# Kernel tuning notes

Hardware: AMD Instinct MI355X
Metric: run time of the kernel (lower is better)

Reference implementation:

```python
import jax, jax.numpy as jnp
import numpy as np

N_PRO = 100000
N_LIG = 100000
E = 500000
H = 128
CE = 18


def _lin_params(key, out_dim, in_dim, scale=0.02):
    kw, kb = jax.random.split(key)
    W = jax.random.normal(kw, (out_dim, in_dim), jnp.float32) * scale
    b = jax.random.normal(kb, (out_dim,), jnp.float32) * scale
    return W, b


def setup_inputs() -> dict:
    key = jax.random.key(0)
    ks = jax.random.split(key, 16)
    inp = {}
    inp['pro_x'] = jax.random.normal(ks[0], (N_PRO, H), jnp.float32)
    inp['lig_x'] = jax.random.normal(ks[1], (N_LIG, H), jnp.float32)
    pi = jax.random.randint(ks[2], (E,), 0, N_PRO)
    li = jax.random.randint(ks[3], (E,), 0, N_LIG)
    inp['cross_ei'] = jnp.stack([pi, li]).astype(jnp.int64)
    inp['cross_ea'] = jax.random.normal(ks[4], (E, CE), jnp.float32)
    inp['Wq_pro'], inp['bq_pro'] = _lin_params(ks[5], H, H)
    inp['Wk_lig'], inp['bk_lig'] = _lin_params(ks[6], H, H)
    inp['Wv_lig'], inp['bv_lig'] = _lin_params(ks[7], H, H)
    inp['Wq_lig'], inp['bq_lig'] = _lin_params(ks[8], H, H)
    inp['Wk_pro'], inp['bk_pro'] = _lin_params(ks[9], H, H)
    inp['Wv_pro'], inp['bv_pro'] = _lin_params(ks[10], H, H)
    inp['We_bias'] = jax.random.normal(ks[11], (CE,), jnp.float32) * 0.02  # Linear(CE,1,bias=False) weight
    inp['Wo_pro'], inp['bo_pro'] = _lin_params(ks[12], H, H)
    inp['Wo_lig'], inp['bo_lig'] = _lin_params(ks[13], H, H)
    inp['g_pro'] = jnp.ones((H,), jnp.float32)
    inp['be_pro'] = jnp.zeros((H,), jnp.float32)
    inp['g_lig'] = jnp.ones((H,), jnp.float32)
    inp['be_lig'] = jnp.zeros((H,), jnp.float32)
    return inp


def _layernorm(x, g, b, eps=1e-5):
    mu = jnp.mean(x, -1, keepdims=True)
    var = jnp.var(x, -1, keepdims=True)
    return (x - mu) * jax.lax.rsqrt(var + eps) * g + b


def _lin(x, W, b):
    return x @ W.T + b


def _attend(Q_src, K_tgt, V_tgt, bias, tgt_idx, n_tgt, scale):
    # per-edge score -> edge softmax over target nodes -> weighted scatter-add
    scores = jnp.sum(Q_src * K_tgt, -1) * scale + bias          # [E]
    scores = scores - jnp.max(scores)                            # global max, as in torch code
    exp_s = jnp.exp(scores)
    denom = jax.ops.segment_sum(exp_s, tgt_idx, num_segments=n_tgt)
    w = exp_s / (denom[tgt_idx] + 1e-8)                          # [E]
    return jax.ops.segment_sum(w[:, None] * V_tgt, tgt_idx, num_segments=n_tgt)  # [n_tgt, H]


def reference(pro_x, lig_x, cross_ei, cross_ea,
              Wq_pro, bq_pro, Wk_lig, bk_lig, Wv_lig, bv_lig,
              Wq_lig, bq_lig, Wk_pro, bk_pro, Wv_pro, bv_pro,
              We_bias, Wo_pro, bo_pro, Wo_lig, bo_lig,
              g_pro, be_pro, g_lig, be_lig):
    pi = cross_ei[0]
    li = cross_ei[1]
    h = pro_x.shape[1]
    scale = h ** (-0.5)
    bias = cross_ea @ We_bias                                    # [E]

    # protein <- ligand
    Qp = _lin(pro_x, Wq_pro, bq_pro)[pi]
    Kl = _lin(lig_x, Wk_lig, bk_lig)[li]
    Vl = _lin(lig_x, Wv_lig, bv_lig)[li]
    pro_upd = _attend(Qp, Kl, Vl, bias, pi, pro_x.shape[0], scale)
    pro_new = _layernorm(pro_x + _lin(pro_upd, Wo_pro, bo_pro), g_pro, be_pro)

    # ligand <- protein
    Ql = _lin(lig_x, Wq_lig, bq_lig)[li]
    Kp = _lin(pro_x, Wk_pro, bk_pro)[pi]
    Vp = _lin(pro_x, Wv_pro, bv_pro)[pi]
    lig_upd = _attend(Ql, Kp, Vp, bias, li, lig_x.shape[0], scale)
    lig_new = _layernorm(lig_x + _lin(lig_upd, Wo_lig, bo_lig), g_lig, be_lig)

    return (pro_new, lig_new)
```

## Files before the change

kernel.cpp:

```cpp
#include <hip/hip_runtime.h>
#include <float.h>
#include <math.h>


typedef __bf16 bf16x8 __attribute__((ext_vector_type(8)));
typedef float  f32x4  __attribute__((ext_vector_type(4)));
typedef float  f32x2  __attribute__((ext_vector_type(2)));
typedef unsigned int u32x2 __attribute__((ext_vector_type(2)));

__device__ __forceinline__ bf16x8 cvt8(const float* p) {
    f32x4 lo = *reinterpret_cast<const f32x4*>(p);
    f32x4 hi = *reinterpret_cast<const f32x4*>(p + 4);
    bf16x8 r;
    r[0] = (__bf16)lo[0]; r[1] = (__bf16)lo[1]; r[2] = (__bf16)lo[2]; r[3] = (__bf16)lo[3];
    r[4] = (__bf16)hi[0]; r[5] = (__bf16)hi[1]; r[6] = (__bf16)hi[2]; r[7] = (__bf16)hi[3];
    return r;
}

__device__ __forceinline__ u32x2 pack_fp8x8(const float* v) {
    int w0 = __builtin_amdgcn_cvt_pk_fp8_f32(v[0], v[1], 0, false);
    w0 = __builtin_amdgcn_cvt_pk_fp8_f32(v[2], v[3], w0, true);
    int w1 = __builtin_amdgcn_cvt_pk_fp8_f32(v[4], v[5], 0, false);
    w1 = __builtin_amdgcn_cvt_pk_fp8_f32(v[6], v[7], w1, true);
    u32x2 r; r[0] = (unsigned)w0; r[1] = (unsigned)w1;
    return r;
}

__device__ __forceinline__ void unpack_fp8x8(u32x2 p, float* out) {
    f32x2 t0 = __builtin_amdgcn_cvt_pk_f32_fp8((int)p[0], false);
    f32x2 t1 = __builtin_amdgcn_cvt_pk_f32_fp8((int)p[0], true);
    f32x2 t2 = __builtin_amdgcn_cvt_pk_f32_fp8((int)p[1], false);
    f32x2 t3 = __builtin_amdgcn_cvt_pk_f32_fp8((int)p[1], true);
    out[0] = t0[0]; out[1] = t0[1]; out[2] = t1[0]; out[3] = t1[1];
    out[4] = t2[0]; out[5] = t2[1]; out[6] = t3[0]; out[7] = t3[1];
}

__device__ __forceinline__ void stage_w512(const __bf16* __restrict__ Ws, char* wlds, int tid) {
#pragma unroll
    for (int it = 0; it < 4; ++it) {
        int idx = it * 4096 + tid * 8;
        int byteoff = idx * 2;
        int row = byteoff >> 8;
        *reinterpret_cast<bf16x8*>(wlds + (byteoff ^ ((row & 7) << 4)))
            = *reinterpret_cast<const bf16x8*>(Ws + idx);
    }
}
__device__ __forceinline__ bf16x8 read_w(const char* wlds, int l15, int lg, int ni, int ks) {
    int row = ni * 16 + l15;
    int off = (row * 256 + ks * 64 + lg * 16) ^ ((row & 7) << 4);
    return *reinterpret_cast<const bf16x8*>(wlds + off);
}

__global__ __launch_bounds__(256) void cvt_weights(
    const float* w0, const float* w1, const float* w2, const float* w3,
    const float* w4, const float* w5, const float* w6, const float* w7,
    __bf16* __restrict__ dst)
{
    const float* srcs[8] = {w0, w1, w2, w3, w4, w5, w6, w7};
    int t = blockIdx.x * 256 + threadIdx.x;
    int mat = t >> 11;
    int base = (t & 2047) * 8;
    const float* s = srcs[mat];
    bool perm = (mat == 3) || (mat == 7);
    __bf16* d = dst + (size_t)mat * 16384;
#pragma unroll
    for (int u = 0; u < 8; ++u) {
        int idx = base + u;
        int row = idx >> 7, c = idx & 127;
        int pos = perm ? ((c & 15) * 8 + (c >> 4)) : c;
        d[row * 128 + pos] = (__bf16)s[idx];
    }
}

__global__ __launch_bounds__(256) void bias_count(
    const float* __restrict__ ea, const float* __restrict__ We,
    const int* __restrict__ pi, const int* __restrict__ li,
    float* __restrict__ bias, int* __restrict__ counts,
    unsigned* __restrict__ ranks, int Np, int E, int CE)
{
    int e = blockIdx.x * 256 + threadIdx.x;
    if (e >= E) return;
    const float2* row = reinterpret_cast<const float2*>(ea + (size_t)e * CE);
    float acc = 0.f;
    int h = CE >> 1;
    for (int c = 0; c < h; ++c) {
        float2 v = row[c];
        acc += v.x * We[2 * c] + v.y * We[2 * c + 1];
    }
    if (CE & 1) acc += ea[(size_t)e * CE + CE - 1] * We[CE - 1];
    bias[e] = acc;
    int r0 = atomicAdd(&counts[pi[e]], 1);
    int r1 = atomicAdd(&counts[Np + li[e]], 1);
    ranks[e] = (unsigned)(r0 & 0xFFFF) | ((unsigned)r1 << 16);
}

__global__ __launch_bounds__(256) void scan1(
    const int* __restrict__ counts, int* __restrict__ offs,
    int* __restrict__ bsums, int N)
{
    int idx = blockIdx.x * 256 + threadIdx.x;
    int v = (idx < N) ? counts[idx] : 0;
    int lane = threadIdx.x & 63, w = threadIdx.x >> 6;
    int x = v;
#pragma unroll
    for (int d = 1; d < 64; d <<= 1) {
        int y = __shfl_up(x, d);
        if (lane >= d) x += y;
    }
    __shared__ int wsum[4];
    if (lane == 63) wsum[w] = x;
    __syncthreads();
    int add = 0;
    for (int i = 0; i < w; ++i) add += wsum[i];
    x += add;
    if (idx < N) offs[idx] = x - v;
    if (threadIdx.x == 255) bsums[blockIdx.x] = x;
}

__global__ __launch_bounds__(1024) void scan2(int* __restrict__ bsums, int nb)
{
    __shared__ int tmp[1024];
    int t = threadIdx.x;
    tmp[t] = (t < nb) ? bsums[t] : 0;
    __syncthreads();
    for (int d = 1; d < 1024; d <<= 1) {
        int y = (t >= d) ? tmp[t - d] : 0;
        __syncthreads();
        tmp[t] += y;
        __syncthreads();
    }
    if (t < nb) bsums[t] = tmp[t];
}

__global__ __launch_bounds__(256) void scan3(
    int* __restrict__ offs, const int* __restrict__ bsums, int N, int total)
{
    int idx = blockIdx.x * 256 + threadIdx.x;
    if (idx < N && blockIdx.x > 0) offs[idx] += bsums[blockIdx.x - 1];
    if (idx == 0) offs[N] = total;
}

__global__ __launch_bounds__(256) void fill2(
    const int* __restrict__ pi, const int* __restrict__ li,
    const float* __restrict__ bias, const unsigned* __restrict__ ranks,
    const int* __restrict__ offs, unsigned* __restrict__ elist, int Np, int E)
{
    int e = blockIdx.x * 256 + threadIdx.x;
    if (e >= E) return;
    int p = pi[e], l = li[e];
    unsigned rk = ranks[e];
    int w = __builtin_amdgcn_cvt_pk_fp8_f32(bias[e], 0.f, 0, false);
    unsigned b8 = (unsigned)w & 0xFFu;
    elist[offs[p] + (rk & 0xFFFFu)]      = ((unsigned)l << 8) | b8;
    elist[offs[Np + l] + (rk >> 16)]     = ((unsigned)p << 8) | b8;
}

__global__ __launch_bounds__(512) void proj3both(
    const float* __restrict__ Xp, const float* __restrict__ Xl,
    const __bf16* __restrict__ W16,
    const float* __restrict__ bq_p, const float* __restrict__ bk_p, const float* __restrict__ bv_p,
    const float* __restrict__ bq_l, const float* __restrict__ bk_l, const float* __restrict__ bv_l,
    char* __restrict__ QKVp, char* __restrict__ QKVl,
    int Np, int Nl, int nbp)
{
    __shared__ char wlds[32768];
    int bid = blockIdx.x;
    int tid = threadIdx.x;
    int lane = tid & 63, wv = tid >> 6;
    int l15 = lane & 15, lg = (lane >> 4) & 3;

    const float* A; const __bf16* Wms[3];
    const float* bsels[3]; char* QKV; int M, wrow;
    if (bid < nbp) {
        A = Xp; M = Np; wrow = bid * 128 + wv * 16;
        Wms[0] = W16 + 0 * 16384; Wms[1] = W16 + 5 * 16384; Wms[2] = W16 + 6 * 16384;
        bsels[0] = bq_p; bsels[1] = bk_p; bsels[2] = bv_p; QKV = QKVp;
    } else {
        A = Xl; M = Nl; wrow = (bid - nbp) * 128 + wv * 16;
        Wms[0] = W16 + 4 * 16384; Wms[1] = W16 + 1 * 16384; Wms[2] = W16 + 2 * 16384;
        bsels[0] = bq_l; bsels[1] = bk_l; bsels[2] = bv_l; QKV = QKVl;
    }
    int r0 = wrow + l15; if (r0 > M - 1) r0 = M - 1;
    const float* Arow0 = A + (size_t)r0 * 128 + lg * 8;

    bf16x8 a0[4];
#pragma unroll
    for (int ks = 0; ks < 4; ++ks) a0[ks] = cvt8(Arow0 + ks * 32);

#pragma unroll
    for (int mat = 0; mat < 3; ++mat) {
        __syncthreads();
        stage_w512(Wms[mat], wlds, tid);
        __syncthreads();

        f32x4 acc[8] = {};
#pragma unroll
        for (int ks = 0; ks < 4; ++ks) {
#pragma unroll
            for (int ni = 0; ni < 8; ++ni)
                acc[ni] = __builtin_amdgcn_mfma_f32_16x16x32_bf16(
                    a0[ks], read_w(wlds, l15, lg, ni, ks), acc[ni], 0, 0, 0);
        }
        float bc[8];
#pragma unroll
        for (int ni = 0; ni < 8; ++ni) bc[ni] = bsels[mat][ni * 16 + l15];
#pragma unroll
        for (int r = 0; r < 4; ++r) {
            int row = wrow + lg * 4 + r;
            if (row < M) {
                float v[8];
#pragma unroll
                for (int ni = 0; ni < 8; ++ni) v[ni] = acc[ni][r] + bc[ni];
                char* rowb = QKV + (size_t)row * 512;
                if (mat == 0) {
                    bf16x8 o;
#pragma unroll
                    for (int ni = 0; ni < 8; ++ni) o[ni] = (__bf16)v[ni];
                    *reinterpret_cast<bf16x8*>(rowb + l15 * 16) = o;
                } else {
                    *reinterpret_cast<u32x2*>(rowb + 256 + (mat - 1) * 128 + l15 * 8)
                        = pack_fp8x8(v);
                }
            }
        }
    }
}

__global__ __launch_bounds__(256) void attend(
    const char* __restrict__ QKVp, const char* __restrict__ QKVl,
    const unsigned* __restrict__ elist, const int* __restrict__ offs,
    __bf16* __restrict__ upd_pro, __bf16* __restrict__ upd_lig,
    int Np, int Ntot, float scale)
{
    int node = blockIdx.x * 16 + (threadIdx.x >> 4);
    if (node >= Ntot) return;
    int l = threadIdx.x & 15;
    const char* Qrow; const char* KV; __bf16* upd;
    if (node < Np) {
        Qrow = QKVp + (size_t)node * 512; KV = QKVl;
        upd = upd_pro + (size_t)node * 128;
    } else {
        int n = node - Np;
        Qrow = QKVl + (size_t)n * 512; KV = QKVp;
        upd = upd_lig + (size_t)n * 128;
    }
    bf16x8 qv = *reinterpret_cast<const bf16x8*>(Qrow + l * 16);
    float q[8];
#pragma unroll
    for (int j = 0; j < 8; ++j) q[j] = (float)qv[j];

    int beg = offs[node], end = offs[node + 1];
    float d = 0.f;
    float acc[8] = {};
    for (int i = beg; i < end; ++i) {
        unsigned rec = elist[i];
        const char* row = KV + (size_t)(rec >> 8) * 512;
        f32x2 bt = __builtin_amdgcn_cvt_pk_f32_fp8((int)(rec & 0xFFu), false);
        u32x2 kk = *reinterpret_cast<const u32x2*>(row + 256 + l * 8);
        u32x2 vp = *reinterpret_cast<const u32x2*>(row + 384 + l * 8);
        float kf[8], vf[8];
        unpack_fp8x8(kk, kf);
        unpack_fp8x8(vp, vf);
        float dot = 0.f;
#pragma unroll
        for (int j = 0; j < 8; ++j) dot += q[j] * kf[j];
#pragma unroll
        for (int t = 1; t < 16; t <<= 1) dot += __shfl_xor(dot, t, 16);
        float s = fminf(dot * scale + bt[0], 60.f);
        float p = __expf(s);
        d += p;
#pragma unroll
        for (int j = 0; j < 8; ++j) acc[j] += p * vf[j];
    }
    float inv = 1.f / (d + 1e-8f);
    bf16x8 o;
#pragma unroll
    for (int j = 0; j < 8; ++j) o[j] = (__bf16)(acc[j] * inv);
    *reinterpret_cast<bf16x8*>(upd + l * 8) = o;
}

__global__ __launch_bounds__(512) void gemm_ln_both(
    const __bf16* __restrict__ upd_pro, const __bf16* __restrict__ upd_lig,
    const float* __restrict__ Xp, const float* __restrict__ Xl,
    const __bf16* __restrict__ W16,
    const float* __restrict__ bo_p, const float* __restrict__ g_p, const float* __restrict__ be_p,
    const float* __restrict__ bo_l, const float* __restrict__ g_l, const float* __restrict__ be_l,
    float* __restrict__ out_pro, float* __restrict__ out_lig,
    int Np, int Nl, int nbp)
{
    __shared__ char wlds[32768];
    int bid = blockIdx.x;
    int tid = threadIdx.x;
    int lane = tid & 63, wv = tid >> 6;
    int l15 = lane & 15, lg = (lane >> 4) & 3;

    const __bf16* A; const float* X; const __bf16* Wo;
    const float *b, *g, *be_; float* C; int M, wrow;
    if (bid < nbp) {
        A = upd_pro; X = Xp; Wo = W16 + 3 * 16384;
        b = bo_p; g = g_p; be_ = be_p; C = out_pro; M = Np; wrow = bid * 128 + wv * 16;
    } else {
        A = upd_lig; X = Xl; Wo = W16 + 7 * 16384;
        b = bo_l; g = g_l; be_ = be_l; C = out_lig; M = Nl; wrow = (bid - nbp) * 128 + wv * 16;
    }
    stage_w512(Wo, wlds, tid);

    int r0 = wrow + l15; if (r0 > M - 1) r0 = M - 1;
    const __bf16* Arow0 = A + (size_t)r0 * 128 + lg * 8;
    bf16x8 a0[4];
#pragma unroll
    for (int ks = 0; ks < 4; ++ks)
        a0[ks] = *reinterpret_cast<const bf16x8*>(Arow0 + ks * 32);
    __syncthreads();

    f32x4 acc[8] = {};
#pragma unroll
    for (int ks = 0; ks < 4; ++ks) {
#pragma unroll
        for (int ni = 0; ni < 8; ++ni)
            acc[ni] = __builtin_amdgcn_mfma_f32_16x16x32_bf16(
                a0[ks], read_w(wlds, l15, lg, ni, ks), acc[ni], 0, 0, 0);
    }

    float bcol[8], gcol[8], becol[8];
#pragma unroll
    for (int ni = 0; ni < 8; ++ni) {
        bcol[ni]  = b[ni * 16 + l15];
        gcol[ni]  = g[ni * 16 + l15];
        becol[ni] = be_[ni * 16 + l15];
    }

#pragma unroll
    for (int r = 0; r < 4; ++r) {
        int row = wrow + lg * 4 + r;
        bool ok = row < M;
        int rowc = ok ? row : M - 1;
        float v[8];
#pragma unroll
        for (int ni = 0; ni < 8; ++ni) v[ni] = acc[ni][r] + bcol[ni];
        const float* Xr = X + (size_t)rowc * 128 + l15;
        float s1 = 0.f, s2 = 0.f;
#pragma unroll
        for (int ni = 0; ni < 8; ++ni) {
            v[ni] += Xr[ni * 16];
            s1 += v[ni]; s2 += v[ni] * v[ni];
        }
#pragma unroll
        for (int d = 1; d < 16; d <<= 1) {
            s1 += __shfl_xor(s1, d);
            s2 += __shfl_xor(s2, d);
        }
        float mu = s1 * 0.0078125f;
        float var = s2 * 0.0078125f - mu * mu;
        float rstd = rsqrtf(var + 1e-5f);
        if (ok) {
            float* Cr = C + (size_t)row * 128 + l15;
#pragma unroll
            for (int ni = 0; ni < 8; ++ni)
                Cr[ni * 16] = (v[ni] - mu) * rstd * gcol[ni] + becol[ni];
        }
    }
}

static inline int cdiv(int a, int b) { return (a + b - 1) / b; }

extern "C" void kernel_launch(void* const* d_in, const int* in_sizes, int n_in,
                              void* d_out, int out_size, void* d_ws, size_t ws_size,
                              hipStream_t stream)
{
    const float* pro_x  = (const float*)d_in[0];
    const float* lig_x  = (const float*)d_in[1];
    const int*   ei     = (const int*)d_in[2];
    const float* ea     = (const float*)d_in[3];
    const float* Wq_pro = (const float*)d_in[4];  const float* bq_pro = (const float*)d_in[5];
    const float* Wk_lig = (const float*)d_in[6];  const float* bk_lig = (const float*)d_in[7];
    const float* Wv_lig = (const float*)d_in[8];  const float* bv_lig = (const float*)d_in[9];
    const float* Wq_lig = (const float*)d_in[10]; const float* bq_lig = (const float*)d_in[11];
    const float* Wk_pro = (const float*)d_in[12]; const float* bk_pro = (const float*)d_in[13];
    const float* Wv_pro = (const float*)d_in[14]; const float* bv_pro = (const float*)d_in[15];
    const float* We     = (const float*)d_in[16];
    const float* Wo_pro = (const float*)d_in[17]; const float* bo_pro = (const float*)d_in[18];
    const float* Wo_lig = (const float*)d_in[19]; const float* bo_lig = (const float*)d_in[20];
    const float* g_pro  = (const float*)d_in[21]; const float* be_pro = (const float*)d_in[22];
    const float* g_lig  = (const float*)d_in[23]; const float* be_lig = (const float*)d_in[24];

    const int Np = in_sizes[0] / 128;
    const int Nl = in_sizes[1] / 128;
    const int E  = in_sizes[2] / 2;
    const int CE = in_sizes[3] / E;
    const int Nmax = Np > Nl ? Np : Nl;
    const int Ntot = Np + Nl;
    const int* pi = ei;
    const int* li = ei + E;

    float* out_pro = (float*)d_out;
    float* out_lig = out_pro + (size_t)Np * 128;

    float* ws = (float*)d_ws;
    size_t o = 0;
    char* QKVp = (char*)(ws + o); o += (size_t)Nmax * 128;
    char* QKVl = (char*)(ws + o); o += (size_t)Nmax * 128;
    float* bias = ws + o;   o += (size_t)E;
    unsigned* ranks = (unsigned*)(ws + o); o += (size_t)E;
    unsigned* elist = (unsigned*)(ws + o); o += 2 * (size_t)E;
    int* counts = (int*)(ws + o); o += (size_t)Ntot + 8;
    int* offs   = (int*)(ws + o); o += (size_t)Ntot + 8;
    int* bsums  = (int*)(ws + o); o += 4096;
    __bf16* W16 = (__bf16*)(ws + o); o += 8 * 16384 / 2;
    __bf16* upd = (__bf16*)(ws + o); o += (size_t)Ntot * 64;
    __bf16* upd_pro = upd;
    __bf16* upd_lig = upd + (size_t)Np * 128;
    (void)ws_size; (void)n_in; (void)out_size;

    const float scale = 1.0f / sqrtf(128.0f);
    const int nEB = cdiv(E, 256);

    (void)hipMemsetAsync(counts, 0, (size_t)(Ntot + 1) * sizeof(int), stream);
    cvt_weights<<<64, 256, 0, stream>>>(Wq_pro, Wk_lig, Wv_lig, Wo_pro,
                                        Wq_lig, Wk_pro, Wv_pro, Wo_lig, W16);
    bias_count<<<nEB, 256, 0, stream>>>(ea, We, pi, li, bias, counts, ranks, Np, E, CE);

    const int nb1 = cdiv(Ntot, 256);
    scan1<<<nb1, 256, 0, stream>>>(counts, offs, bsums, Ntot);
    scan2<<<1, 1024, 0, stream>>>(bsums, nb1);
    scan3<<<nb1, 256, 0, stream>>>(offs, bsums, Ntot, 2 * E);
    fill2<<<nEB, 256, 0, stream>>>(pi, li, bias, ranks, offs, elist, Np, E);

    const int nbp = cdiv(Np, 128), nbl = cdiv(Nl, 128);
    proj3both<<<nbp + nbl, 512, 0, stream>>>(pro_x, lig_x, W16,
        bq_pro, bk_pro, bv_pro, bq_lig, bk_lig, bv_lig,
        QKVp, QKVl, Np, Nl, nbp);

    attend<<<cdiv(Ntot, 16), 256, 0, stream>>>(QKVp, QKVl, elist, offs,
        upd_pro, upd_lig, Np, Ntot, scale);

    gemm_ln_both<<<nbp + nbl, 512, 0, stream>>>(upd_pro, upd_lig,
        pro_x, lig_x, W16, bo_pro, g_pro, be_pro, bo_lig, g_lig, be_lig,
        out_pro, out_lig, Np, Nl, nbp);
}
```

Before: 265.3 us.

## Retile QKV projection per-wave without LDS weight staging

```diff
diff --git a/kernel.cpp b/kernel.cpp
--- a/kernel.cpp
+++ b/kernel.cpp
@@ -4,6 +4,7 @@
 
 
 typedef __bf16 bf16x8 __attribute__((ext_vector_type(8)));
+typedef __bf16 bf16x4 __attribute__((ext_vector_type(4)));
 typedef float  f32x4  __attribute__((ext_vector_type(4)));
 typedef float  f32x2  __attribute__((ext_vector_type(2)));
 typedef unsigned int u32x2 __attribute__((ext_vector_type(2)));
@@ -17,13 +18,10 @@
     return r;
 }
 
-__device__ __forceinline__ u32x2 pack_fp8x8(const float* v) {
-    int w0 = __builtin_amdgcn_cvt_pk_fp8_f32(v[0], v[1], 0, false);
-    w0 = __builtin_amdgcn_cvt_pk_fp8_f32(v[2], v[3], w0, true);
-    int w1 = __builtin_amdgcn_cvt_pk_fp8_f32(v[4], v[5], 0, false);
-    w1 = __builtin_amdgcn_cvt_pk_fp8_f32(v[6], v[7], w1, true);
-    u32x2 r; r[0] = (unsigned)w0; r[1] = (unsigned)w1;
-    return r;
+__device__ __forceinline__ unsigned pack_fp8x4(const float* v) {
+    int w = __builtin_amdgcn_cvt_pk_fp8_f32(v[0], v[1], 0, false);
+    w = __builtin_amdgcn_cvt_pk_fp8_f32(v[2], v[3], w, true);
+    return (unsigned)w;
 }
 
 __device__ __forceinline__ void unpack_fp8x8(u32x2 p, float* out) {
@@ -161,65 +159,85 @@
     const float* __restrict__ bq_p, const float* __restrict__ bk_p, const float* __restrict__ bv_p,
     const float* __restrict__ bq_l, const float* __restrict__ bk_l, const float* __restrict__ bv_l,
     char* __restrict__ QKVp, char* __restrict__ QKVl,
-    int Np, int Nl, int nbp)
-{
-    __shared__ char wlds[32768];
-    int bid = blockIdx.x;
-    int tid = threadIdx.x;
-    int lane = tid & 63, wv = tid >> 6;
+    int Np, int Nl, int nwp, int nwtot)
+{
+    int gw = blockIdx.x * 8 + (threadIdx.x >> 6);
+    if (gw >= nwtot) return;
+    int lane = threadIdx.x & 63;
     int l15 = lane & 15, lg = (lane >> 4) & 3;
 
     const float* A; const __bf16* Wms[3];
-    const float* bsels[3]; char* QKV; int M, wrow;
-    if (bid < nbp) {
-        A = Xp; M = Np; wrow = bid * 128 + wv * 16;
+    const float* bsels[3]; char* QKV; int M, rowbase, cg;
+    if (gw < nwp) {
+        A = Xp; M = Np; rowbase = (gw >> 1) * 32; cg = gw & 1;
         Wms[0] = W16 + 0 * 16384; Wms[1] = W16 + 5 * 16384; Wms[2] = W16 + 6 * 16384;
         bsels[0] = bq_p; bsels[1] = bk_p; bsels[2] = bv_p; QKV = QKVp;
     } else {
-        A = Xl; M = Nl; wrow = (bid - nbp) * 128 + wv * 16;
+        int g = gw - nwp;
+        A = Xl; M = Nl; rowbase = (g >> 1) * 32; cg = g & 1;
         Wms[0] = W16 + 4 * 16384; Wms[1] = W16 + 1 * 16384; Wms[2] = W16 + 2 * 16384;
         bsels[0] = bq_l; bsels[1] = bk_l; bsels[2] = bv_l; QKV = QKVl;
     }
-    int r0 = wrow + l15; if (r0 > M - 1) r0 = M - 1;
+    if (rowbase >= M) return;
+
+    int r0 = rowbase + l15;      if (r0 > M - 1) r0 = M - 1;
+    int r1 = rowbase + 16 + l15; if (r1 > M - 1) r1 = M - 1;
     const float* Arow0 = A + (size_t)r0 * 128 + lg * 8;
-
-    bf16x8 a0[4];
-#pragma unroll
-    for (int ks = 0; ks < 4; ++ks) a0[ks] = cvt8(Arow0 + ks * 32);
+    const float* Arow1 = A + (size_t)r1 * 128 + lg * 8;
+
+    bf16x8 a0[4], a1[4];
+#pragma unroll
+    for (int ks = 0; ks < 4; ++ks) {
+        a0[ks] = cvt8(Arow0 + ks * 32);
+        a1[ks] = cvt8(Arow1 + ks * 32);
+    }
 
 #pragma unroll
     for (int mat = 0; mat < 3; ++mat) {
-        __syncthreads();
-        stage_w512(Wms[mat], wlds, tid);
-        __syncthreads();
-
-        f32x4 acc[8] = {};
+        const __bf16* Wsel = Wms[mat];
+        const __bf16* Wb = Wsel + ((size_t)(cg * 4) * 16 + l15) * 128 + lg * 8;
+
+        f32x4 acc0[4] = {}, acc1[4] = {};
 #pragma unroll
         for (int ks = 0; ks < 4; ++ks) {
-#pragma unroll
-            for (int ni = 0; ni < 8; ++ni)
-                acc[ni] = __builtin_amdgcn_mfma_f32_16x16x32_bf16(
-                    a0[ks], read_w(wlds, l15, lg, ni, ks), acc[ni], 0, 0, 0);
+            bf16x8 w0 = *reinterpret_cast<const bf16x8*>(Wb + 0 * 2048 + ks * 32);
+            bf16x8 w1 = *reinterpret_cast<const bf16x8*>(Wb + 1 * 2048 + ks * 32);
+            bf16x8 w2 = *reinterpret_cast<const bf16x8*>(Wb + 2 * 2048 + ks * 32);
+            bf16x8 w3 = *reinterpret_cast<const bf16x8*>(Wb + 3 * 2048 + ks * 32);
+            acc0[0] = __builtin_amdgcn_mfma_f32_16x16x32_bf16(a0[ks], w0, acc0[0], 0, 0, 0);
+            acc1[0] = __builtin_amdgcn_mfma_f32_16x16x32_bf16(a1[ks], w0, acc1[0], 0, 0, 0);
+            acc0[1] = __builtin_amdgcn_mfma_f32_16x16x32_bf16(a0[ks], w1, acc0[1], 0, 0, 0);
+            acc1[1] = __builtin_amdgcn_mfma_f32_16x16x32_bf16(a1[ks], w1, acc1[1], 0, 0, 0);
+            acc0[2] = __builtin_amdgcn_mfma_f32_16x16x32_bf16(a0[ks], w2, acc0[2], 0, 0, 0);
+            acc1[2] = __builtin_amdgcn_mfma_f32_16x16x32_bf16(a1[ks], w2, acc1[2], 0, 0, 0);
+            acc0[3] = __builtin_amdgcn_mfma_f32_16x16x32_bf16(a0[ks], w3, acc0[3], 0, 0, 0);
+            acc1[3] = __builtin_amdgcn_mfma_f32_16x16x32_bf16(a1[ks], w3, acc1[3], 0, 0, 0);
         }
-        float bc[8];
-#pragma unroll
-        for (int ni = 0; ni < 8; ++ni) bc[ni] = bsels[mat][ni * 16 + l15];
-#pragma unroll
-        for (int r = 0; r < 4; ++r) {
-            int row = wrow + lg * 4 + r;
-            if (row < M) {
-                float v[8];
-#pragma unroll
-                for (int ni = 0; ni < 8; ++ni) v[ni] = acc[ni][r] + bc[ni];
-                char* rowb = QKV + (size_t)row * 512;
-                if (mat == 0) {
-                    bf16x8 o;
-#pragma unroll
-                    for (int ni = 0; ni < 8; ++ni) o[ni] = (__bf16)v[ni];
-                    *reinterpret_cast<bf16x8*>(rowb + l15 * 16) = o;
-                } else {
-                    *reinterpret_cast<u32x2*>(rowb + 256 + (mat - 1) * 128 + l15 * 8)
-                        = pack_fp8x8(v);
+
+        float bc[4];
+#pragma unroll
+        for (int ni = 0; ni < 4; ++ni) bc[ni] = bsels[mat][(cg * 4 + ni) * 16 + l15];
+
+#pragma unroll
+        for (int mi = 0; mi < 2; ++mi) {
+#pragma unroll
+            for (int r = 0; r < 4; ++r) {
+                int row = rowbase + mi * 16 + lg * 4 + r;
+                if (row < M) {
+                    float v[4];
+#pragma unroll
+                    for (int ni = 0; ni < 4; ++ni)
+                        v[ni] = (mi == 0 ? acc0[ni][r] : acc1[ni][r]) + bc[ni];
+                    char* rowb = QKV + (size_t)row * 512;
+                    if (mat == 0) {
+                        bf16x4 o;
+#pragma unroll
+                        for (int ni = 0; ni < 4; ++ni) o[ni] = (__bf16)v[ni];
+                        *reinterpret_cast<bf16x4*>(rowb + l15 * 16 + cg * 8) = o;
+                    } else {
+                        *reinterpret_cast<unsigned*>(rowb + 256 + (mat - 1) * 128 + l15 * 8 + cg * 4)
+                            = pack_fp8x4(v);
+                    }
                 }
             }
         }
@@ -426,14 +444,16 @@
     scan3<<<nb1, 256, 0, stream>>>(offs, bsums, Ntot, 2 * E);
     fill2<<<nEB, 256, 0, stream>>>(pi, li, bias, ranks, offs, elist, Np, E);
 
-    const int nbp = cdiv(Np, 128), nbl = cdiv(Nl, 128);
-    proj3both<<<nbp + nbl, 512, 0, stream>>>(pro_x, lig_x, W16,
+    const int nwp = cdiv(Np, 32) * 2, nwl = cdiv(Nl, 32) * 2;
+    const int nwtot = nwp + nwl;
+    proj3both<<<cdiv(nwtot, 8), 512, 0, stream>>>(pro_x, lig_x, W16,
         bq_pro, bk_pro, bv_pro, bq_lig, bk_lig, bv_lig,
-        QKVp, QKVl, Np, Nl, nbp);
+        QKVp, QKVl, Np, Nl, nwp, nwtot);
 
     attend<<<cdiv(Ntot, 16), 256, 0, stream>>>(QKVp, QKVl, elist, offs,
         upd_pro, upd_lig, Np, Ntot, scale);
 
+    const int nbp = cdiv(Np, 128), nbl = cdiv(Nl, 128);
     gemm_ln_both<<<nbp + nbl, 512, 0, stream>>>(upd_pro, upd_lig,
         pro_x, lig_x, W16, bo_pro, g_pro, be_pro, bo_lig, g_lig, be_lig,
         out_pro, out_lig, Np, Nl, nbp);
```

Result: slower. 339.0 us (+27.8%).
